# Kernel optimization log

Measured on AMD Instinct MI355X. Metric: run time of the kernel, lower is better.

## Reference

```python
import jax, jax.numpy as jnp
from jax import lax
import numpy as np

B, S, T = 32, 512, 64
IN, H, L, HC, OUT = 512, 512, 2, 4, 512

def setup_inputs() -> dict:
    key = jax.random.key(0)
    ks = jax.random.split(key, 12)
    def w(k, shape, fan_in):
        return (jax.random.normal(k, shape, jnp.float32) / np.float32(np.sqrt(fan_in)))
    lstm_in0 = IN + HC * H
    return {
        "inputs": jax.random.normal(ks[0], (B, T, IN), jnp.float32),
        "lengths": jax.random.randint(ks[1], (B,), 1, S + 1),
        "final_hiddens": jax.random.normal(ks[2], (L, B, H), jnp.float32),
        "hiddens": jax.random.normal(ks[3], (B, S, H), jnp.float32),
        "max_output_len": T,
        "max_seq_len": S,
        "Wa1": w(ks[4], (H, 2 * H), 2 * H), "ba1": jnp.zeros((H,), jnp.float32),
        "Wa2": w(ks[5], (HC, H), H), "ba2": jnp.zeros((HC,), jnp.float32),
        "W_ih0": w(ks[6], (4 * H, lstm_in0), lstm_in0), "W_hh0": w(ks[7], (4 * H, H), H),
        "b_ih0": jnp.zeros((4 * H,), jnp.float32), "b_hh0": jnp.zeros((4 * H,), jnp.float32),
        "W_ih1": w(ks[8], (4 * H, H), H), "W_hh1": w(ks[9], (4 * H, H), H),
        "b_ih1": jnp.zeros((4 * H,), jnp.float32), "b_hh1": jnp.zeros((4 * H,), jnp.float32),
        "Wo1": w(ks[10], (H, (1 + HC) * H), (1 + HC) * H), "bo1": jnp.zeros((H,), jnp.float32),
        "Wo2": w(ks[11], (OUT, H), H), "bo2": jnp.zeros((OUT,), jnp.float32),
    }

def _lstm_cell(x, h, c, W_ih, W_hh, b_ih, b_hh):
    # PyTorch LSTM gate order: i, f, g, o
    g = x @ W_ih.T + b_ih + h @ W_hh.T + b_hh
    i, f, gg, o = jnp.split(g, 4, axis=-1)
    c_new = jax.nn.sigmoid(f) * c + jax.nn.sigmoid(i) * jnp.tanh(gg)
    h_new = jax.nn.sigmoid(o) * jnp.tanh(c_new)
    return h_new, c_new

def reference(inputs, lengths, final_hiddens, hiddens, max_output_len, max_seq_len,
              Wa1, ba1, Wa2, ba2, W_ih0, W_hh0, b_ih0, b_hh0,
              W_ih1, W_hh1, b_ih1, b_hh1, Wo1, bo1, Wo2, bo2):
    batch = inputs.shape[0]
    # r_mask[b, s] = 1 if s < lengths[b] else 0  -> [B, S, 1]
    r_mask = (jnp.arange(max_seq_len)[None, :] < lengths[:, None]).astype(hiddens.dtype)[..., None]

    def step(carry, x_t):
        h, c = carry  # each [L, B, H]
        last = h[-1]  # [B, H]
        dup = last[:, None, :] * r_mask  # [B, S, H]
        a = jax.nn.relu(jnp.concatenate([dup, hiddens], axis=2) @ Wa1.T + ba1)  # [B,S,H]
        a = jax.nn.relu(a @ Wa2.T + ba2)  # [B,S,HC]
        a = jax.nn.softmax(a, axis=1)  # softmax over seq dim (unmasked, as in source)
        c_vecs = jnp.einsum('bsk,bsh->bkh', a, hiddens).reshape(batch, -1)  # [B, HC*H]
        x = jnp.concatenate([x_t, c_vecs], axis=1)  # [B, IN + HC*H]
        h0, c0 = _lstm_cell(x, h[0], c[0], W_ih0, W_hh0, b_ih0, b_hh0)
        h1, c1 = _lstm_cell(h0, h[1], c[1], W_ih1, W_hh1, b_ih1, b_hh1)
        out = jnp.tanh(jax.nn.relu(jnp.concatenate([h1, c_vecs], axis=1) @ Wo1.T + bo1) @ Wo2.T + bo2)
        return (jnp.stack([h0, h1]), jnp.stack([c0, c1])), out

    c_init = jnp.zeros_like(final_hiddens)
    _, outs = lax.scan(step, (final_hiddens, c_init), jnp.swapaxes(inputs, 0, 1))  # [T,B,OUT]
    return jnp.swapaxes(outs, 0, 1)  # [B, T, OUT]
```

## Files before the change

### kernel.cpp

```cpp
#include <hip/hip_runtime.h>
#include <cmath>


typedef unsigned short ushort;
typedef unsigned int uint;
typedef __attribute__((ext_vector_type(8))) short bf16x8;
typedef __attribute__((ext_vector_type(4))) float f32x4;

__device__ __forceinline__ float sigmoidf_(float x) { return 1.f / (1.f + __expf(-x)); }
__device__ __forceinline__ float bf2f(ushort u) {
  union { uint i; float f; } x; x.i = ((uint)u) << 16; return x.f;
}
__device__ __forceinline__ ushort f2bf(float f) {
  union { float f; uint i; } x; x.f = f;
  return (ushort)((x.i + 0x7FFFu + ((x.i >> 16) & 1u)) >> 16);
}
__device__ __forceinline__ float wave_sum(float v) {
#pragma unroll
  for (int m = 1; m < 64; m <<= 1) v += __shfl_xor(v, m, 64);
  return v;
}
__device__ __forceinline__ float wave_max(float v) {
#pragma unroll
  for (int m = 1; m < 64; m <<= 1) v = fmaxf(v, __shfl_xor(v, m, 64));
  return v;
}

__global__ void __launch_bounds__(256) k_init(const float* __restrict__ fh,
                                              ushort* h0b0, ushort* h1b0,
                                              float* c0, float* c1) {
  int i = blockIdx.x * 256 + threadIdx.x;
  h0b0[i] = f2bf(fh[i]);
  h1b0[i] = f2bf(fh[16384 + i]);
  c0[i] = 0.f; c1[i] = 0.f;
}

__global__ void __launch_bounds__(256) k_prep(const float* __restrict__ hid,
                                              ushort* __restrict__ hbf) {
  size_t i0 = ((size_t)blockIdx.x * 256 + threadIdx.x) * 8;
  float4 f0 = *(const float4*)&hid[i0];
  float4 f1 = *(const float4*)&hid[i0 + 4];
  uint4 o;
  o.x = (uint)f2bf(f0.x) | ((uint)f2bf(f0.y) << 16);
  o.y = (uint)f2bf(f0.z) | ((uint)f2bf(f0.w) << 16);
  o.z = (uint)f2bf(f1.x) | ((uint)f2bf(f1.y) << 16);
  o.w = (uint)f2bf(f1.z) | ((uint)f2bf(f1.w) << 16);
  *(uint4*)&hbf[i0] = o;
}

__global__ void __launch_bounds__(256) k_inprep(const float* __restrict__ inputs,
                                                ushort* __restrict__ inb) {
  size_t idx4 = ((size_t)blockIdx.x * 256 + threadIdx.x) * 4;
  int m = (int)(idx4 >> 9), k = (int)(idx4 & 511);
  int b = m & 31, tt = m >> 5;
  float4 v = *(const float4*)&inputs[((size_t)b * 64 + tt) * 512 + k];
  ushort4 o; o.x = f2bf(v.x); o.y = f2bf(v.y); o.z = f2bf(v.z); o.w = f2bf(v.w);
  *(ushort4*)&inb[(size_t)m * 512 + k] = o;
}

__global__ void __launch_bounds__(256) k_wcvt(const float* __restrict__ W1, int ld1,
                                              const float* __restrict__ W2, int ld2,
                                              int split, int K,
                                              ushort* __restrict__ dst) {
  size_t idx = ((size_t)blockIdx.x * 256 + threadIdx.x) * 4;
  int j = (int)(idx / K), k = (int)(idx % K);
  const float* src = (k < split) ? (W1 + (size_t)j * ld1 + k)
                                 : (W2 + (size_t)j * ld2 + (k - split));
  float4 v = *(const float4*)src;
  ushort4 o; o.x = f2bf(v.x); o.y = f2bf(v.y); o.z = f2bf(v.z); o.w = f2bf(v.w);
  *(ushort4*)&dst[idx] = o;
}

__global__ void __launch_bounds__(256) k_hidproj(const float* __restrict__ hid,
                                                 const float* __restrict__ Wa1,
                                                 ushort* __restrict__ hpT) {
  __shared__ float As[64][33];
  __shared__ float Bs[64][33];
  int tid = threadIdx.x;
  int r0 = blockIdx.x * 64;
  int n0 = blockIdx.y * 64;
  int b = r0 >> 9, sb = r0 & 511;
  int tm = (tid >> 4) << 2, tn = (tid & 15) << 2;
  int lr = tid >> 2, lk = (tid & 3) << 3;
  float acc[4][4] = {};
  for (int k0 = 0; k0 < 512; k0 += 32) {
    float4 a0 = *(const float4*)&hid[(size_t)(r0 + lr) * 512 + k0 + lk];
    float4 a1 = *(const float4*)&hid[(size_t)(r0 + lr) * 512 + k0 + lk + 4];
    float4 b0 = *(const float4*)&Wa1[(size_t)(n0 + lr) * 1024 + 512 + k0 + lk];
    float4 b1 = *(const float4*)&Wa1[(size_t)(n0 + lr) * 1024 + 512 + k0 + lk + 4];
    __syncthreads();
    As[lr][lk+0]=a0.x; As[lr][lk+1]=a0.y; As[lr][lk+2]=a0.z; As[lr][lk+3]=a0.w;
    As[lr][lk+4]=a1.x; As[lr][lk+5]=a1.y; As[lr][lk+6]=a1.z; As[lr][lk+7]=a1.w;
    Bs[lr][lk+0]=b0.x; Bs[lr][lk+1]=b0.y; Bs[lr][lk+2]=b0.z; Bs[lr][lk+3]=b0.w;
    Bs[lr][lk+4]=b1.x; Bs[lr][lk+5]=b1.y; Bs[lr][lk+6]=b1.z; Bs[lr][lk+7]=b1.w;
    __syncthreads();
#pragma unroll 8
    for (int kk = 0; kk < 32; kk++) {
      float av[4], bv[4];
#pragma unroll
      for (int i = 0; i < 4; i++) av[i] = As[tm + i][kk];
#pragma unroll
      for (int j = 0; j < 4; j++) bv[j] = Bs[tn + j][kk];
#pragma unroll
      for (int i = 0; i < 4; i++)
#pragma unroll
        for (int j = 0; j < 4; j++) acc[i][j] += av[i] * bv[j];
    }
  }
#pragma unroll
  for (int j = 0; j < 4; j++) {
    ushort4 o;
    o.x = f2bf(acc[0][j]); o.y = f2bf(acc[1][j]);
    o.z = f2bf(acc[2][j]); o.w = f2bf(acc[3][j]);
    *(ushort4*)&hpT[((size_t)b * 512 + n0 + tn + j) * 512 + sb + tm] = o;
  }
}

__global__ void __launch_bounds__(512) k_scst(const ushort* __restrict__ hpT,
                                              const float* __restrict__ ba1,
                                              const float* __restrict__ Wa2,
                                              float4* __restrict__ scoresP4) {
  int bid = blockIdx.x, tid = threadIdx.x;
  int b = bid >> 3, kdq = bid & 7, kd0 = kdq << 6, s = tid;
  float a0 = 0.f, a1 = 0.f, a2 = 0.f, a3 = 0.f;
  const ushort* hpr = hpT + ((size_t)b * 512 + kd0) * 512 + s;
#pragma unroll 4
  for (int i = 0; i < 64; i++) {
    int kd = kd0 + i;
    float a = fmaxf(bf2f(hpr[(size_t)i * 512]) + ba1[kd], 0.f);
    a0 += Wa2[kd] * a;
    a1 += Wa2[512 + kd] * a;
    a2 += Wa2[1024 + kd] * a;
    a3 += Wa2[1536 + kd] * a;
  }
  scoresP4[((size_t)(kdq * 32 + b)) * 512 + s] = make_float4(a0, a1, a2, a3);
}

__global__ void __launch_bounds__(512) k_sum0(const float4* __restrict__ scoresP4,
                                              const float* __restrict__ ba2,
                                              float* __restrict__ scores0) {
  int idx = blockIdx.x * 512 + threadIdx.x;
  int b = idx >> 9, s = idx & 511;
  float a0 = ba2[0], a1 = ba2[1], a2 = ba2[2], a3 = ba2[3];
#pragma unroll
  for (int q = 0; q < 8; q++) {
    float4 p = scoresP4[((size_t)(q * 32 + b)) * 512 + s];
    a0 += p.x; a1 += p.y; a2 += p.z; a3 += p.w;
  }
  scores0[((size_t)b * 4 + 0) * 512 + s] = fmaxf(a0, 0.f);
  scores0[((size_t)b * 4 + 1) * 512 + s] = fmaxf(a1, 0.f);
  scores0[((size_t)b * 4 + 2) * 512 + s] = fmaxf(a2, 0.f);
  scores0[((size_t)b * 4 + 3) * 512 + s] = fmaxf(a3, 0.f);
}

__global__ void __launch_bounds__(512) k_stat0(const float* __restrict__ scores0,
                                               const int* __restrict__ lengths,
                                               float* __restrict__ m0v,
                                               float* __restrict__ statZ,
                                               float* __restrict__ P0) {
  __shared__ float st[32], st2[32];
  int b = blockIdx.x, tid = threadIdx.x, lane = tid & 63, w = tid >> 6;
  int s = tid, len = lengths[b];
  bool stat = s >= len;
  float v[4], m0[4];
#pragma unroll
  for (int k = 0; k < 4; k++) v[k] = scores0[((size_t)b * 4 + k) * 512 + s];
#pragma unroll
  for (int k = 0; k < 4; k++) {
    float mk = wave_max(stat ? v[k] : -1e30f);
    if (lane == 0) st[w * 4 + k] = mk;
  }
  __syncthreads();
#pragma unroll
  for (int k = 0; k < 4; k++) {
    float m = st[k];
#pragma unroll
    for (int w2 = 1; w2 < 8; w2++) m = fmaxf(m, st[w2 * 4 + k]);
    m0[k] = m;
  }
  float e[4];
#pragma unroll
  for (int k = 0; k < 4; k++) {
    e[k] = stat ? __expf(v[k] - m0[k]) : 0.f;
    float sk = wave_sum(e[k]);
    if (lane == 0) st2[w * 4 + k] = sk;
  }
  __syncthreads();
#pragma unroll
  for (int k = 0; k < 4; k++) {
    P0[((size_t)b * 4 + k) * 512 + s] = e[k];
  }
  if (tid == 0) {
#pragma unroll
    for (int k = 0; k < 4; k++) {
      float z = 0.f;
#pragma unroll
      for (int w2 = 0; w2 < 8; w2++) z += st2[w2 * 4 + k];
      m0v[b * 4 + k] = m0[k];
      statZ[b * 4 + k] = z;
    }
  }
}

__global__ void __launch_bounds__(512) k_statvec(const float* __restrict__ P0,
                                                 const ushort* __restrict__ hbf,
                                                 const int* __restrict__ lengths,
                                                 float* __restrict__ statvec) {
  __shared__ float P[4 * 512];
  __shared__ float red2[8 * 256];
  int bid = blockIdx.x, tid = threadIdx.x;
  int b = bid >> 3, hs = bid & 7;
#pragma unroll
  for (int k = 0; k < 4; k++) P[k * 512 + tid] = P0[((size_t)b * 4 + k) * 512 + tid];
  __syncthreads();
  int h = tid & 63, w8 = tid >> 6;
  int len = lengths[b];
  float a0 = 0.f, a1 = 0.f, a2 = 0.f, a3 = 0.f;
  for (int si = len + ((w8 - len) & 7); si < 512; si += 8) {
    float hv = bf2f(hbf[((size_t)(b * 512 + si) * 512) + (hs << 6) + h]);
    a0 += P[si] * hv;
    a1 += P[512 + si] * hv;
    a2 += P[1024 + si] * hv;
    a3 += P[1536 + si] * hv;
  }
  red2[(w8 << 8) + h] = a0;
  red2[(w8 << 8) + 64 + h] = a1;
  red2[(w8 << 8) + 128 + h] = a2;
  red2[(w8 << 8) + 192 + h] = a3;
  __syncthreads();
  if (tid < 256) {
    int k = tid >> 6, hh = tid & 63;
    float acc = 0.f;
#pragma unroll
    for (int c = 0; c < 8; c++) acc += red2[(c << 8) + (k << 6) + hh];
    statvec[((size_t)b * 4 + k) * 512 + (hs << 6) + hh] = acc;
  }
}

__device__ __forceinline__ void mfma_slice(
    const ushort* __restrict__ W, int ldW, int jrow0, int jstride,
    const ushort* __restrict__ xA, int ldA, int xsplit,
    const ushort* __restrict__ xB, int ldB, int coff,
    int klo, int khi, float* __restrict__ redrow) {
  const int l = threadIdx.x & 63;
  const int r16 = l & 15, koff = (l >> 4) * 8;
  const int j = jrow0 + (r16 & 3) + (r16 >> 2) * jstride;
  const ushort* wrow = W + (size_t)j * ldW + koff;
  const ushort* a0A = xA + (size_t)r16 * ldA + koff;
  const ushort* a1A = xA + (size_t)(16 + r16) * ldA + koff;
  const ushort* a0B = xB + (size_t)r16 * ldB + koff;
  const ushort* a1B = xB + (size_t)(16 + r16) * ldB + koff;
  f32x4 acc0 = {0.f, 0.f, 0.f, 0.f}, acc1 = {0.f, 0.f, 0.f, 0.f};
#pragma unroll 4
  for (int k0 = klo; k0 < khi; k0 += 32) {
    bf16x8 av0, av1;
    if (k0 < xsplit) {
      av0 = *(const bf16x8*)(a0A + k0);
      av1 = *(const bf16x8*)(a1A + k0);
    } else {
      av0 = *(const bf16x8*)(a0B + (k0 - coff));
      av1 = *(const bf16x8*)(a1B + (k0 - coff));
    }
    bf16x8 wv = *(const bf16x8*)(wrow + k0);
    acc0 = __builtin_amdgcn_mfma_f32_16x16x32_bf16(av0, wv, acc0, 0, 0, 0);
    acc1 = __builtin_amdgcn_mfma_f32_16x16x32_bf16(av1, wv, acc1, 0, 0, 0);
  }
  const int brow = (l >> 4) << 2;
#pragma unroll
  for (int r = 0; r < 4; r++) {
    redrow[r16 * 33 + brow + r] = acc0[r];
    redrow[r16 * 33 + 16 + brow + r] = acc1[r];
  }
}

__global__ void __launch_bounds__(256) k_gin0(const ushort* __restrict__ Wg0b,
                                              const ushort* __restrict__ inb,
                                              float* __restrict__ gi0) {
  __shared__ float red[4 * 528];
  int tid = threadIdx.x, w = tid >> 6;
  int j0 = blockIdx.x * 16;
  for (int mt = 0; mt < 4; mt++) {
    int m0 = (blockIdx.y * 4 + mt) * 32;
    mfma_slice(Wg0b, 3072, j0, 4, inb + (size_t)m0 * 512, 512, 1 << 30,
               inb + (size_t)m0 * 512, 512, 0, w * 128, w * 128 + 128,
               red + w * 528);
    __syncthreads();
#pragma unroll
    for (int e = 0; e < 2; e++) {
      int idx = tid + e * 256;
      int j = idx >> 5, b = idx & 31;
      float v = 0.f;
#pragma unroll
      for (int ww = 0; ww < 4; ww++) v += red[ww * 528 + j * 33 + b];
      gi0[(size_t)(m0 + b) * 2048 + j0 + j] = v;
    }
    __syncthreads();
  }
}

__global__ void __launch_bounds__(512) k_scq(
    const ushort* __restrict__ Wq, const ushort* __restrict__ Wo1,
    const ushort* __restrict__ h1cur, const ushort* __restrict__ xb,
    const float* __restrict__ bo1, ushort* __restrict__ o1bf,
    const ushort* __restrict__ hpT, const float* __restrict__ ba1,
    const float* __restrict__ Wa2, const int* __restrict__ lengths,
    float4* __restrict__ scoresP4, int t) {
  __shared__ float red[8 * 528];
  __shared__ float qs[64];
  int bid = blockIdx.x, tid = threadIdx.x, w = tid >> 6, lane = tid & 63;
  if (bid < 32) {
    if (t < 1) return;
    mfma_slice(Wo1, 2560, bid * 16, 4, h1cur, 512, 512, xb, 2048, 512,
               w * 320, w * 320 + 320, red + w * 528);
    __syncthreads();
    int j = tid & 15, b = tid >> 4;
    float v = 0.f;
#pragma unroll
    for (int ww = 0; ww < 8; ww++) v += red[ww * 528 + j * 33 + b];
    int jj = bid * 16 + j;
    o1bf[b * 512 + jj] = f2bf(fmaxf(v + bo1[jj], 0.f));
  } else {
    if (t >= 64) return;
    int r = bid - 32;
    int b = r >> 3, kdq = r & 7, kd0 = kdq << 6;
    {
      bf16x8 hv8 = *(const bf16x8*)(h1cur + b * 512 + lane * 8);
      float hf[8];
#pragma unroll
      for (int e2 = 0; e2 < 8; e2++) hf[e2] = bf2f(((ushort*)&hv8)[e2]);
#pragma unroll
      for (int rr = 0; rr < 8; rr++) {
        int row = kd0 + w * 8 + rr;
        bf16x8 wv8 = *(const bf16x8*)(Wq + (size_t)row * 512 + lane * 8);
        float acc = 0.f;
#pragma unroll
        for (int e2 = 0; e2 < 8; e2++) acc += hf[e2] * bf2f(((ushort*)&wv8)[e2]);
        acc = wave_sum(acc);
        if (lane == 0) qs[w * 8 + rr] = acc;
      }
    }
    __syncthreads();
    int s = tid, len = lengths[b];
    if ((tid & ~63) >= len) return;
    float m = (s < len) ? 1.f : 0.f;
    float a0 = 0.f, a1 = 0.f, a2 = 0.f, a3 = 0.f;
    const ushort* hpr = hpT + ((size_t)b * 512 + kd0) * 512 + s;
#pragma unroll 4
    for (int i = 0; i < 64; i++) {
      int kd = kd0 + i;
      float hv = bf2f(hpr[(size_t)i * 512]);
      float a = fmaxf(hv + ba1[kd] + m * qs[i], 0.f);
      a0 += Wa2[kd] * a;
      a1 += Wa2[512 + kd] * a;
      a2 += Wa2[1024 + kd] * a;
      a3 += Wa2[1536 + kd] * a;
    }
    scoresP4[((size_t)(kdq * 32 + b)) * 512 + s] = make_float4(a0, a1, a2, a3);
  }
}

__global__ void __launch_bounds__(512) k_ctxout(
    const float4* __restrict__ scoresP4, const float* __restrict__ ba2,
    const int* __restrict__ lengths, const ushort* __restrict__ hbf,
    const float* __restrict__ m0v, const float* __restrict__ statZ,
    const float* __restrict__ statvec, ushort* __restrict__ xb,
    const ushort* __restrict__ Wo2, const ushort* __restrict__ o1bf,
    const float* __restrict__ bo2, float* __restrict__ outp, int t) {
  __shared__ float red[8 * 528];
  __shared__ float P[4 * 512];
  __shared__ float red2[8 * 256];
  __shared__ float st[32], st2[32];
  int bid = blockIdx.x, tid = threadIdx.x;
  if (bid < 32) {
    if (t < 1) return;
    int w = tid >> 6;
    mfma_slice(Wo2, 512, bid * 16, 4, o1bf, 512, 1 << 30, o1bf, 512, 0,
               w * 64, w * 64 + 64, red + w * 528);
    __syncthreads();
    int j = tid & 15, b = tid >> 4;
    float v = 0.f;
#pragma unroll
    for (int ww = 0; ww < 8; ww++) v += red[ww * 528 + j * 33 + b];
    int jj = bid * 16 + j;
    outp[((size_t)b * 64 + (t - 1)) * 512 + jj] = tanhf(v + bo2[jj]);
  } else {
    if (t >= 64) return;
    int r = bid - 32;
    int b = r >> 3, hs = r & 7;
    int lane = tid & 63, w = tid >> 6;
    int s = tid, len = lengths[b];
    bool act = s < len;
    float v[4];
    {
      float a0 = ba2[0], a1 = ba2[1], a2 = ba2[2], a3 = ba2[3];
      if (act) {
#pragma unroll
        for (int q = 0; q < 8; q++) {
          float4 p = scoresP4[((size_t)(q * 32 + b)) * 512 + s];
          a0 += p.x; a1 += p.y; a2 += p.z; a3 += p.w;
        }
        v[0] = fmaxf(a0, 0.f); v[1] = fmaxf(a1, 0.f);
        v[2] = fmaxf(a2, 0.f); v[3] = fmaxf(a3, 0.f);
      } else {
        v[0] = v[1] = v[2] = v[3] = -1e30f;
      }
    }
    float M[4];
#pragma unroll
    for (int k = 0; k < 4; k++) {
      float mk = wave_max(v[k]);
      if (lane == 0) st[w * 4 + k] = mk;
    }
    __syncthreads();
#pragma unroll
    for (int k = 0; k < 4; k++) {
      float m = st[k];
#pragma unroll
      for (int w2 = 1; w2 < 8; w2++) m = fmaxf(m, st[w2 * 4 + k]);
      M[k] = fmaxf(m, m0v[b * 4 + k]);
    }
    float e[4];
#pragma unroll
    for (int k = 0; k < 4; k++) {
      e[k] = act ? __expf(v[k] - M[k]) : 0.f;
      float sk = wave_sum(e[k]);
      if (lane == 0) st2[w * 4 + k] = sk;
    }
    __syncthreads();
    float sc[4];
#pragma unroll
    for (int k = 0; k < 4; k++) {
      float dynZ = 0.f;
#pragma unroll
      for (int w2 = 0; w2 < 8; w2++) dynZ += st2[w2 * 4 + k];
      float scB = __expf(m0v[b * 4 + k] - M[k]);
      float Z = dynZ + scB * statZ[b * 4 + k];
      float invZ = 1.f / Z;
      P[k * 512 + s] = e[k] * invZ;
      sc[k] = scB * invZ;
    }
    __syncthreads();
    int h = tid & 63, w8 = tid >> 6;
    float a0 = 0.f, a1 = 0.f, a2 = 0.f, a3 = 0.f;
    const ushort* hb0 = hbf + ((size_t)b * 512) * 512 + (hs << 6) + h;
    for (int si = w8; si < len; si += 8) {
      float hv = bf2f(hb0[(size_t)si * 512]);
      a0 += P[si] * hv;
      a1 += P[512 + si] * hv;
      a2 += P[1024 + si] * hv;
      a3 += P[1536 + si] * hv;
    }
    red2[(w8 << 8) + h] = a0;
    red2[(w8 << 8) + 64 + h] = a1;
    red2[(w8 << 8) + 128 + h] = a2;
    red2[(w8 << 8) + 192 + h] = a3;
    __syncthreads();
    if (tid < 256) {
      int k = tid >> 6, hh = tid & 63;
      float acc = 0.f;
#pragma unroll
      for (int c = 0; c < 8; c++) acc += red2[(c << 8) + (k << 6) + hh];
      acc += sc[k] * statvec[((size_t)b * 4 + k) * 512 + (hs << 6) + hh];
      xb[b * 2048 + (k << 9) + (hs << 6) + hh] = f2bf(acc);
    }
  }
}

__global__ void __launch_bounds__(512) k_cell0(
    const ushort* __restrict__ Wg0b, const ushort* __restrict__ xb,
    const ushort* __restrict__ h0cur, const float* __restrict__ gi0,
    const float* __restrict__ bih, const float* __restrict__ bhh,
    float* __restrict__ cst, ushort* __restrict__ hnew, int t) {
  __shared__ float red[8 * 528];
  int bid = blockIdx.x, tid = threadIdx.x, w = tid >> 6;
  mfma_slice(Wg0b + 512, 3072, bid * 4, 512, xb, 2048, 2048, h0cur, 512, 2048,
             w * 320, w * 320 + 320, red + w * 528);
  __syncthreads();
  if (tid < 128) {
    int b = tid & 31, dh = tid >> 5;
    int h = bid * 4 + dh;
    float G[4];
#pragma unroll
    for (int g = 0; g < 4; g++) {
      float v = bih[g * 512 + h] + bhh[g * 512 + h] +
                gi0[(size_t)(t * 32 + b) * 2048 + g * 512 + h];
#pragma unroll
      for (int ww = 0; ww < 8; ww++) v += red[ww * 528 + (g * 4 + dh) * 33 + b];
      G[g] = v;
    }
    float i_ = sigmoidf_(G[0]), f_ = sigmoidf_(G[1]);
    float gg = tanhf(G[2]), o_ = sigmoidf_(G[3]);
    float cn = f_ * cst[b * 512 + h] + i_ * gg;
    cst[b * 512 + h] = cn;
    hnew[b * 512 + h] = f2bf(o_ * tanhf(cn));
  }
}

__global__ void __launch_bounds__(512) k_cell1(
    const ushort* __restrict__ Wg1b, const ushort* __restrict__ h0new,
    const ushort* __restrict__ h1cur, const float* __restrict__ bih,
    const float* __restrict__ bhh, float* __restrict__ cst,
    ushort* __restrict__ hnew) {
  __shared__ float red[8 * 528];
  int bid = blockIdx.x, tid = threadIdx.x, w = tid >> 6;
  mfma_slice(Wg1b, 1024, bid * 4, 512, h0new, 512, 512, h1cur, 512, 512,
             w * 128, w * 128 + 128, red + w * 528);
  __syncthreads();
  if (tid < 128) {
    int b = tid & 31, dh = tid >> 5;
    int h = bid * 4 + dh;
    float G[4];
#pragma unroll
    for (int g = 0; g < 4; g++) {
      float v = bih[g * 512 + h] + bhh[g * 512 + h];
#pragma unroll
      for (int ww = 0; ww < 8; ww++) v += red[ww * 528 + (g * 4 + dh) * 33 + b];
      G[g] = v;
    }
    float i_ = sigmoidf_(G[0]), f_ = sigmoidf_(G[1]);
    float gg = tanhf(G[2]), o_ = sigmoidf_(G[3]);
    float cn = f_ * cst[b * 512 + h] + i_ * gg;
    cst[b * 512 + h] = cn;
    hnew[b * 512 + h] = f2bf(o_ * tanhf(cn));
  }
}

extern "C" void kernel_launch(void* const* d_in, const int* in_sizes, int n_in,
                              void* d_out, int out_size, void* d_ws, size_t ws_size,
                              hipStream_t stream) {
  const float* inputs  = (const float*)d_in[0];
  const int*   lengths = (const int*)d_in[1];
  const float* fh      = (const float*)d_in[2];
  const float* hiddens = (const float*)d_in[3];
  const float* Wa1  = (const float*)d_in[6];
  const float* ba1  = (const float*)d_in[7];
  const float* Wa2  = (const float*)d_in[8];
  const float* ba2  = (const float*)d_in[9];
  const float* Wih0 = (const float*)d_in[10];
  const float* Whh0 = (const float*)d_in[11];
  const float* bih0 = (const float*)d_in[12];
  const float* bhh0 = (const float*)d_in[13];
  const float* Wih1 = (const float*)d_in[14];
  const float* Whh1 = (const float*)d_in[15];
  const float* bih1 = (const float*)d_in[16];
  const float* bhh1 = (const float*)d_in[17];
  const float* Wo1  = (const float*)d_in[18];
  const float* bo1  = (const float*)d_in[19];
  const float* Wo2  = (const float*)d_in[20];
  const float* bo2  = (const float*)d_in[21];
  float* outp = (float*)d_out;

  char* p = (char*)d_ws;
  ushort* hpT = (ushort*)p; p += (size_t)32 * 512 * 512 * 2;
  ushort* hbf = (ushort*)p; p += (size_t)32 * 512 * 512 * 2;
  float4* scoresP4 = (float4*)p; p += (size_t)8 * 32 * 512 * 16;
  float* scores0 = (float*)p; p += (size_t)32 * 4 * 512 * 4;
  float* P0      = (float*)p; p += (size_t)32 * 4 * 512 * 4;
  float* statvec = (float*)p; p += (size_t)32 * 4 * 512 * 4;
  float* m0v     = (float*)p; p += 128 * sizeof(float);
  float* statZ   = (float*)p; p += 128 * sizeof(float);
  ushort* xb     = (ushort*)p; p += (size_t)32 * 2048 * 2;
  ushort* h0b    = (ushort*)p; p += (size_t)2 * 32 * 512 * 2;
  ushort* h1b    = (ushort*)p; p += (size_t)2 * 32 * 512 * 2;
  ushort* o1bf   = (ushort*)p; p += (size_t)32 * 512 * 2;
  float* c0      = (float*)p; p += (size_t)32 * 512 * 4;
  float* c1      = (float*)p; p += (size_t)32 * 512 * 4;
  ushort* Wg0b   = (ushort*)p; p += (size_t)2048 * 3072 * 2;
  ushort* Wg1b   = (ushort*)p; p += (size_t)2048 * 1024 * 2;
  ushort* Wo1b   = (ushort*)p; p += (size_t)512 * 2560 * 2;
  ushort* Wo2b   = (ushort*)p; p += (size_t)512 * 512 * 2;
  ushort* Wqb    = (ushort*)p; p += (size_t)512 * 512 * 2;
  ushort* inb    = (ushort*)p; p += (size_t)2048 * 512 * 2;
  float* gi0     = (float*)p; p += (size_t)2048 * 2048 * 4;

  k_init<<<64, 256, 0, stream>>>(fh, h0b, h1b, c0, c1);
  k_prep<<<4096, 256, 0, stream>>>(hiddens, hbf);
  k_inprep<<<1024, 256, 0, stream>>>(inputs, inb);
  k_hidproj<<<dim3(256, 8), 256, 0, stream>>>(hiddens, Wa1, hpT);
  k_wcvt<<<6144, 256, 0, stream>>>(Wih0, 2560, Whh0, 512, 2560, 3072, Wg0b);
  k_wcvt<<<2048, 256, 0, stream>>>(Wih1, 512, Whh1, 512, 512, 1024, Wg1b);
  k_wcvt<<<1280, 256, 0, stream>>>(Wo1, 2560, Wo1, 2560, 2560, 2560, Wo1b);
  k_wcvt<<<256, 256, 0, stream>>>(Wo2, 512, Wo2, 512, 512, 512, Wo2b);
  k_wcvt<<<256, 256, 0, stream>>>(Wa1, 1024, Wa1, 1024, 512, 512, Wqb);
  k_gin0<<<dim3(128, 16), 256, 0, stream>>>(Wg0b, inb, gi0);
  k_scst<<<256, 512, 0, stream>>>(hpT, ba1, Wa2, scoresP4);
  k_sum0<<<32, 512, 0, stream>>>(scoresP4, ba2, scores0);
  k_stat0<<<32, 512, 0, stream>>>(scores0, lengths, m0v, statZ, P0);
  k_statvec<<<256, 512, 0, stream>>>(P0, hbf, lengths, statvec);

  for (int t = 0; t <= 64; t++) {
    const ushort* h1cur = h1b + (size_t)(t & 1) * 16384;
    const ushort* h0cur = h0b + (size_t)(t & 1) * 16384;
    ushort* h0nxt = h0b + (size_t)((t + 1) & 1) * 16384;
    ushort* h1nxt = h1b + (size_t)((t + 1) & 1) * 16384;
    k_scq<<<288, 512, 0, stream>>>(Wqb, Wo1b, h1cur, xb, bo1, o1bf, hpT, ba1,
                                   Wa2, lengths, scoresP4, t);
    k_ctxout<<<288, 512, 0, stream>>>(scoresP4, ba2, lengths, hbf, m0v, statZ,
                                      statvec, xb, Wo2b, o1bf, bo2, outp, t);
    if (t < 64) {
      k_cell0<<<128, 512, 0, stream>>>(Wg0b, xb, h0cur, gi0, bih0, bhh0, c0,
                                       h0nxt, t);
      k_cell1<<<128, 512, 0, stream>>>(Wg1b, h0nxt, h1cur, bih1, bhh1, c1, h1nxt);
    }
  }
}
```

Baseline: 3.597 ms.

## Store hidden projection row-major and vectorize per-thread score accumulation

Changes the precomputed hidden projection from a transposed [b][kd][s] layout to row-major [b][s][kd], so each thread reads its 64 contiguous kd values with 16-byte vector loads instead of strided scalar loads. Wa2 and ba1 slices are staged in shared memory for the per-step score kernel and the startup score kernel. A context-accumulation loop in another kernel is also unrolled by four. The risk is that adjacent threads now read addresses 1KB apart, which loses coalescing across the wave and relies on cache-line reuse over the unrolled vector loads.

New measurement: 2.987 ms. -17.0%, faster.

```diff
diff --git a/kernel.cpp b/kernel.cpp
--- a/kernel.cpp
+++ b/kernel.cpp
@@ -73,13 +73,12 @@
 
 __global__ void __launch_bounds__(256) k_hidproj(const float* __restrict__ hid,
                                                  const float* __restrict__ Wa1,
-                                                 ushort* __restrict__ hpT) {
+                                                 ushort* __restrict__ hpb) {
   __shared__ float As[64][33];
   __shared__ float Bs[64][33];
   int tid = threadIdx.x;
   int r0 = blockIdx.x * 64;
   int n0 = blockIdx.y * 64;
-  int b = r0 >> 9, sb = r0 & 511;
   int tm = (tid >> 4) << 2, tn = (tid & 15) << 2;
   int lr = tid >> 2, lk = (tid & 3) << 3;
   float acc[4][4] = {};
@@ -108,31 +107,49 @@
     }
   }
 #pragma unroll
-  for (int j = 0; j < 4; j++) {
+  for (int i = 0; i < 4; i++) {
     ushort4 o;
-    o.x = f2bf(acc[0][j]); o.y = f2bf(acc[1][j]);
-    o.z = f2bf(acc[2][j]); o.w = f2bf(acc[3][j]);
-    *(ushort4*)&hpT[((size_t)b * 512 + n0 + tn + j) * 512 + sb + tm] = o;
-  }
-}
-
-__global__ void __launch_bounds__(512) k_scst(const ushort* __restrict__ hpT,
+    o.x = f2bf(acc[i][0]); o.y = f2bf(acc[i][1]);
+    o.z = f2bf(acc[i][2]); o.w = f2bf(acc[i][3]);
+    *(ushort4*)&hpb[(size_t)(r0 + tm + i) * 512 + n0 + tn] = o;
+  }
+}
+
+__device__ __forceinline__ void scores_accum(const ushort* __restrict__ hpr,
+                                             const float* __restrict__ wa2s,
+                                             const float* __restrict__ ba1s,
+                                             const float* __restrict__ qs, float m,
+                                             float& a0, float& a1, float& a2,
+                                             float& a3) {
+#pragma unroll
+  for (int i8 = 0; i8 < 8; i8++) {
+    bf16x8 hv8 = *(const bf16x8*)(hpr + i8 * 8);
+#pragma unroll
+    for (int e = 0; e < 8; e++) {
+      int i = i8 * 8 + e;
+      float a = fmaxf(bf2f(((ushort*)&hv8)[e]) + ba1s[i] + m * qs[i], 0.f);
+      a0 += wa2s[i] * a;
+      a1 += wa2s[64 + i] * a;
+      a2 += wa2s[128 + i] * a;
+      a3 += wa2s[192 + i] * a;
+    }
+  }
+}
+
+__global__ void __launch_bounds__(512) k_scst(const ushort* __restrict__ hpb,
                                               const float* __restrict__ ba1,
                                               const float* __restrict__ Wa2,
                                               float4* __restrict__ scoresP4) {
+  __shared__ float wa2s[256], ba1s[64], qz[64];
   int bid = blockIdx.x, tid = threadIdx.x;
   int b = bid >> 3, kdq = bid & 7, kd0 = kdq << 6, s = tid;
+  if (tid < 256) wa2s[tid] = Wa2[(tid >> 6) * 512 + kd0 + (tid & 63)];
+  else if (tid < 320) ba1s[tid - 256] = ba1[kd0 + (tid - 256)];
+  else if (tid < 384) qz[tid - 320] = 0.f;
+  __syncthreads();
   float a0 = 0.f, a1 = 0.f, a2 = 0.f, a3 = 0.f;
-  const ushort* hpr = hpT + ((size_t)b * 512 + kd0) * 512 + s;
-#pragma unroll 4
-  for (int i = 0; i < 64; i++) {
-    int kd = kd0 + i;
-    float a = fmaxf(bf2f(hpr[(size_t)i * 512]) + ba1[kd], 0.f);
-    a0 += Wa2[kd] * a;
-    a1 += Wa2[512 + kd] * a;
-    a2 += Wa2[1024 + kd] * a;
-    a3 += Wa2[1536 + kd] * a;
-  }
+  const ushort* hpr = hpb + (size_t)(b * 512 + s) * 512 + kd0;
+  scores_accum(hpr, wa2s, ba1s, qz, 0.f, a0, a1, a2, a3);
   scoresP4[((size_t)(kdq * 32 + b)) * 512 + s] = make_float4(a0, a1, a2, a3);
 }
 
@@ -302,11 +319,11 @@
     const ushort* __restrict__ Wq, const ushort* __restrict__ Wo1,
     const ushort* __restrict__ h1cur, const ushort* __restrict__ xb,
     const float* __restrict__ bo1, ushort* __restrict__ o1bf,
-    const ushort* __restrict__ hpT, const float* __restrict__ ba1,
+    const ushort* __restrict__ hpb, const float* __restrict__ ba1,
     const float* __restrict__ Wa2, const int* __restrict__ lengths,
     float4* __restrict__ scoresP4, int t) {
   __shared__ float red[8 * 528];
-  __shared__ float qs[64];
+  __shared__ float qs[64], wa2s[256], ba1s[64];
   int bid = blockIdx.x, tid = threadIdx.x, w = tid >> 6, lane = tid & 63;
   if (bid < 32) {
     if (t < 1) return;
@@ -323,6 +340,8 @@
     if (t >= 64) return;
     int r = bid - 32;
     int b = r >> 3, kdq = r & 7, kd0 = kdq << 6;
+    if (tid < 256) wa2s[tid] = Wa2[(tid >> 6) * 512 + kd0 + (tid & 63)];
+    else if (tid < 320) ba1s[tid - 256] = ba1[kd0 + (tid - 256)];
     {
       bf16x8 hv8 = *(const bf16x8*)(h1cur + b * 512 + lane * 8);
       float hf[8];
@@ -344,17 +363,8 @@
     if ((tid & ~63) >= len) return;
     float m = (s < len) ? 1.f : 0.f;
     float a0 = 0.f, a1 = 0.f, a2 = 0.f, a3 = 0.f;
-    const ushort* hpr = hpT + ((size_t)b * 512 + kd0) * 512 + s;
-#pragma unroll 4
-    for (int i = 0; i < 64; i++) {
-      int kd = kd0 + i;
-      float hv = bf2f(hpr[(size_t)i * 512]);
-      float a = fmaxf(hv + ba1[kd] + m * qs[i], 0.f);
-      a0 += Wa2[kd] * a;
-      a1 += Wa2[512 + kd] * a;
-      a2 += Wa2[1024 + kd] * a;
-      a3 += Wa2[1536 + kd] * a;
-    }
+    const ushort* hpr = hpb + (size_t)(b * 512 + s) * 512 + kd0;
+    scores_accum(hpr, wa2s, ba1s, qs, m, a0, a1, a2, a3);
     scoresP4[((size_t)(kdq * 32 + b)) * 512 + s] = make_float4(a0, a1, a2, a3);
   }
 }
@@ -443,7 +453,21 @@
     int h = tid & 63, w8 = tid >> 6;
     float a0 = 0.f, a1 = 0.f, a2 = 0.f, a3 = 0.f;
     const ushort* hb0 = hbf + ((size_t)b * 512) * 512 + (hs << 6) + h;
-    for (int si = w8; si < len; si += 8) {
+    int si = w8;
+    for (; si + 24 < len; si += 32) {
+      float h0v = bf2f(hb0[(size_t)si * 512]);
+      float h1v = bf2f(hb0[(size_t)(si + 8) * 512]);
+      float h2v = bf2f(hb0[(size_t)(si + 16) * 512]);
+      float h3v = bf2f(hb0[(size_t)(si + 24) * 512]);
+      a0 += P[si] * h0v + P[si + 8] * h1v + P[si + 16] * h2v + P[si + 24] * h3v;
+      a1 += P[512 + si] * h0v + P[512 + si + 8] * h1v + P[512 + si + 16] * h2v +
+            P[512 + si + 24] * h3v;
+      a2 += P[1024 + si] * h0v + P[1024 + si + 8] * h1v + P[1024 + si + 16] * h2v +
+            P[1024 + si + 24] * h3v;
+      a3 += P[1536 + si] * h0v + P[1536 + si + 8] * h1v + P[1536 + si + 16] * h2v +
+            P[1536 + si + 24] * h3v;
+    }
+    for (; si < len; si += 8) {
       float hv = bf2f(hb0[(size_t)si * 512]);
       a0 += P[si] * hv;
       a1 += P[512 + si] * hv;
@@ -551,7 +575,7 @@
   float* outp = (float*)d_out;
 
   char* p = (char*)d_ws;
-  ushort* hpT = (ushort*)p; p += (size_t)32 * 512 * 512 * 2;
+  ushort* hpb = (ushort*)p; p += (size_t)32 * 512 * 512 * 2;
   ushort* hbf = (ushort*)p; p += (size_t)32 * 512 * 512 * 2;
   float4* scoresP4 = (float4*)p; p += (size_t)8 * 32 * 512 * 16;
   float* scores0 = (float*)p; p += (size_t)32 * 4 * 512 * 4;
@@ -576,14 +600,14 @@
   k_init<<<64, 256, 0, stream>>>(fh, h0b, h1b, c0, c1);
   k_prep<<<4096, 256, 0, stream>>>(hiddens, hbf);
   k_inprep<<<1024, 256, 0, stream>>>(inputs, inb);
-  k_hidproj<<<dim3(256, 8), 256, 0, stream>>>(hiddens, Wa1, hpT);
+  k_hidproj<<<dim3(256, 8), 256, 0, stream>>>(hiddens, Wa1, hpb);
   k_wcvt<<<6144, 256, 0, stream>>>(Wih0, 2560, Whh0, 512, 2560, 3072, Wg0b);
   k_wcvt<<<2048, 256, 0, stream>>>(Wih1, 512, Whh1, 512, 512, 1024, Wg1b);
   k_wcvt<<<1280, 256, 0, stream>>>(Wo1, 2560, Wo1, 2560, 2560, 2560, Wo1b);
   k_wcvt<<<256, 256, 0, stream>>>(Wo2, 512, Wo2, 512, 512, 512, Wo2b);
   k_wcvt<<<256, 256, 0, stream>>>(Wa1, 1024, Wa1, 1024, 512, 512, Wqb);
   k_gin0<<<dim3(128, 16), 256, 0, stream>>>(Wg0b, inb, gi0);
-  k_scst<<<256, 512, 0, stream>>>(hpT, ba1, Wa2, scoresP4);
+  k_scst<<<256, 512, 0, stream>>>(hpb, ba1, Wa2, scoresP4);
   k_sum0<<<32, 512, 0, stream>>>(scoresP4, ba2, scores0);
   k_stat0<<<32, 512, 0, stream>>>(scores0, lengths, m0v, statZ, P0);
   k_statvec<<<256, 512, 0, stream>>>(P0, hbf, lengths, statvec);
@@ -593,7 +617,7 @@
     const ushort* h0cur = h0b + (size_t)(t & 1) * 16384;
     ushort* h0nxt = h0b + (size_t)((t + 1) & 1) * 16384;
     ushort* h1nxt = h1b + (size_t)((t + 1) & 1) * 16384;
-    k_scq<<<288, 512, 0, stream>>>(Wqb, Wo1b, h1cur, xb, bo1, o1bf, hpT, ba1,
+    k_scq<<<288, 512, 0, stream>>>(Wqb, Wo1b, h1cur, xb, bo1, o1bf, hpb, ba1,
                                    Wa2, lengths, scoresP4, t);
     k_ctxout<<<288, 512, 0, stream>>>(scoresP4, ba2, lengths, hbf, m0v, statZ,
                                       statvec, xb, Wo2b, o1bf, bo2, outp, t);
```
